# Optimization experiments

Hardware: AMD Instinct MI355X
Metric: run time of the kernel (lower is better)

## Reference

```python
import jax, jax.numpy as jnp
import numpy as np

M_CHANNELS = 256
N_KNOTS = 64
EPS = 1e-6


def setup_inputs() -> dict:
    key = jax.random.key(0)
    k_u, k_c = jax.random.split(key)
    u = jax.random.uniform(k_u, (4096, 64, M_CHANNELS), dtype=jnp.float32)
    # knots: per-channel sorted ascending, init linspace(0,1) as in the module
    knots = jnp.tile(jnp.linspace(0.0, 1.0, N_KNOTS, dtype=jnp.float32)[None, :],
                     (M_CHANNELS, 1))
    # coefs init to zeros in the module; use randn for a non-degenerate test
    coefs = jax.random.normal(k_c, (M_CHANNELS, N_KNOTS), dtype=jnp.float32)
    return {"u": u, "knots": knots, "coefs": coefs}


def reference(u, knots, coefs):
    """Piecewise-linear spline eval, vectorized over channels and points.
    u: [..., M], knots/coefs: [M, K] (knots sorted ascending per channel).
    """
    m, K = knots.shape
    orig_shape = u.shape
    flat = u.reshape(-1, m).T  # [M, N]
    # torch.bucketize(right=False) == searchsorted side='left'
    idx = jax.vmap(lambda k, x: jnp.searchsorted(k, x, side='left'))(knots, flat)
    idx0 = jnp.clip(idx - 1, 0, K - 2)  # [M, N]
    idx1 = idx0 + 1
    k0 = jnp.take_along_axis(knots, idx0, axis=1)
    k1 = jnp.take_along_axis(knots, idx1, axis=1)
    c0 = jnp.take_along_axis(coefs, idx0, axis=1)
    c1 = jnp.take_along_axis(coefs, idx1, axis=1)
    t = (flat - k0) / (k1 - k0 + EPS)
    out = c0 + t * (c1 - c0)  # [M, N]
    return out.T.reshape(orig_shape)
```

## Files before the change

### kernel.cpp

```cpp
#include <hip/hip_runtime.h>


#define EPS 1e-6f
#define NCH_GROUP 32
#define STRIDE 65
#define NGROUPS 8
#define BLOCKS_PER_GROUP 256
#define ROWS_PER_TILE 32

typedef float f32x4 __attribute__((ext_vector_type(4)));

__global__ __launch_bounds__(256, 8) void bspline_kernel(
    const float* __restrict__ u, const float* __restrict__ knots,
    const float* __restrict__ coefs, float* __restrict__ out, int n_rows)
{
    __shared__ float sK[NCH_GROUP * STRIDE];
    __shared__ float sC[NCH_GROUP * STRIDE];

    const int t = threadIdx.x;
    const int g = blockIdx.x & (NGROUPS - 1);
    const int b = blockIdx.x >> 3;

    const float* gk = knots + (size_t)g * NCH_GROUP * 64;
    const float* gc = coefs + (size_t)g * NCH_GROUP * 64;
    for (int i = t; i < NCH_GROUP * 64; i += 256) {
        int c = i >> 6;
        int k = i & 63;
        sK[c * STRIDE + k] = gk[i];
        sC[c * STRIDE + k] = gc[i];
    }
    __syncthreads();

    const int col4 = t & 7;
    const int rsub = t >> 3;
    const int lc = col4 * 4;

    float kmin[4], scale[4];
#pragma unroll
    for (int cc = 0; cc < 4; ++cc) {
        float klo = sK[(lc + cc) * STRIDE + 0];
        float khi = sK[(lc + cc) * STRIDE + 63];
        kmin[cc] = klo;
        scale[cc] = 63.0f * __builtin_amdgcn_rcpf(khi - klo);
    }

    const f32x4* u4 = (const f32x4*)u;
    f32x4* o4 = (f32x4*)out;
    const int colbase = g * 8 + col4;
    const int ntiles = n_rows / ROWS_PER_TILE;

    int rt = b;
    if (rt >= ntiles) return;
    size_t idx = (size_t)(rt * ROWS_PER_TILE + rsub) * 64 + colbase;
    f32x4 x4 = __builtin_nontemporal_load(&u4[idx]);

    for (;;) {
        const int rtn = rt + BLOCKS_PER_GROUP;
        const bool more = rtn < ntiles;
        size_t idxn = idx;
        f32x4 xn = x4;
        if (more) {
            idxn = (size_t)(rtn * ROWS_PER_TILE + rsub) * 64 + colbase;
            xn = __builtin_nontemporal_load(&u4[idxn]);
        }

        f32x4 r;
#pragma unroll
        for (int cc = 0; cc < 4; ++cc) {
            float x = x4[cc];
            const float* kp = &sK[(lc + cc) * STRIDE];
            const float* cp = &sC[(lc + cc) * STRIDE];

            float xs = (x - kmin[cc]) * scale[cc];
            int j = (int)xs;
            j = max(0, min(62, j));
            float k0 = kp[j];
            float k1 = kp[j + 1];
            while (j > 0 && k0 >= x) { --j; k1 = k0; k0 = kp[j]; }
            while (j < 62 && k1 < x) { ++j; k0 = k1; k1 = kp[j + 1]; }

            float tt = (x - k0) * __builtin_amdgcn_rcpf(k1 - k0 + EPS);
            float c0 = cp[j];
            float c1 = cp[j + 1];
            r[cc] = fmaf(tt, c1 - c0, c0);
        }
        __builtin_nontemporal_store(r, &o4[idx]);

        if (!more) break;
        rt = rtn; idx = idxn; x4 = xn;
    }
}

extern "C" void kernel_launch(void* const* d_in, const int* in_sizes, int n_in,
                              void* d_out, int out_size, void* d_ws, size_t ws_size,
                              hipStream_t stream) {
    const float* u     = (const float*)d_in[0];
    const float* knots = (const float*)d_in[1];
    const float* coefs = (const float*)d_in[2];
    float* out = (float*)d_out;

    int n_rows = in_sizes[0] / 256;

    dim3 grid(NGROUPS * BLOCKS_PER_GROUP);
    dim3 block(256);
    bspline_kernel<<<grid, block, 0, stream>>>(u, knots, coefs, out, n_rows);
}
```

Baseline: 443.1 us.

## Pack knot/coef segment pairs into float4 LDS and simplify row loop

Shared memory now holds one float4 per segment (k0, k1, c0, c1), so each lookup needs a single 128-bit LDS read instead of four scalar reads. The change also halves the blocks per channel group, drops the occupancy hint in the launch bounds, removes the manual software prefetch of the next tile, and replaces nontemporal loads and stores with ordinary ones. LDS use rises from about 16KB to 32KB per block, which can lower occupancy. The float4 reads with a 64-entry row stride may also cause bank conflicts, and the loop loses its explicit overlap of the next load with the current computation.

After: 450.2 us. Within noise of the previous version (+1.6%).

```diff
diff --git a/kernel.cpp b/kernel.cpp
--- a/kernel.cpp
+++ b/kernel.cpp
@@ -3,19 +3,17 @@
 
 #define EPS 1e-6f
 #define NCH_GROUP 32
-#define STRIDE 65
 #define NGROUPS 8
-#define BLOCKS_PER_GROUP 256
+#define BLOCKS_PER_GROUP 128
 #define ROWS_PER_TILE 32
 
 typedef float f32x4 __attribute__((ext_vector_type(4)));
 
-__global__ __launch_bounds__(256, 8) void bspline_kernel(
+__global__ __launch_bounds__(256) void bspline_kernel(
     const float* __restrict__ u, const float* __restrict__ knots,
     const float* __restrict__ coefs, float* __restrict__ out, int n_rows)
 {
-    __shared__ float sK[NCH_GROUP * STRIDE];
-    __shared__ float sC[NCH_GROUP * STRIDE];
+    __shared__ f32x4 sP[NCH_GROUP * 64];
 
     const int t = threadIdx.x;
     const int g = blockIdx.x & (NGROUPS - 1);
@@ -23,11 +21,15 @@
 
     const float* gk = knots + (size_t)g * NCH_GROUP * 64;
     const float* gc = coefs + (size_t)g * NCH_GROUP * 64;
-    for (int i = t; i < NCH_GROUP * 64; i += 256) {
-        int c = i >> 6;
-        int k = i & 63;
-        sK[c * STRIDE + k] = gk[i];
-        sC[c * STRIDE + k] = gc[i];
+    for (int i = t; i < NCH_GROUP * 63; i += 256) {
+        int c = i / 63;
+        int j = i - c * 63;
+        f32x4 p;
+        p.x = gk[c * 64 + j];
+        p.y = gk[c * 64 + j + 1];
+        p.z = gc[c * 64 + j];
+        p.w = gc[c * 64 + j + 1];
+        sP[(c << 6) + j] = p;
     }
     __syncthreads();
 
@@ -38,8 +40,8 @@
     float kmin[4], scale[4];
 #pragma unroll
     for (int cc = 0; cc < 4; ++cc) {
-        float klo = sK[(lc + cc) * STRIDE + 0];
-        float khi = sK[(lc + cc) * STRIDE + 63];
+        float klo = sP[(lc + cc) << 6].x;
+        float khi = sP[((lc + cc) << 6) + 62].y;
         kmin[cc] = klo;
         scale[cc] = 63.0f * __builtin_amdgcn_rcpf(khi - klo);
     }
@@ -49,45 +51,27 @@
     const int colbase = g * 8 + col4;
     const int ntiles = n_rows / ROWS_PER_TILE;
 
-    int rt = b;
-    if (rt >= ntiles) return;
-    size_t idx = (size_t)(rt * ROWS_PER_TILE + rsub) * 64 + colbase;
-    f32x4 x4 = __builtin_nontemporal_load(&u4[idx]);
-
-    for (;;) {
-        const int rtn = rt + BLOCKS_PER_GROUP;
-        const bool more = rtn < ntiles;
-        size_t idxn = idx;
-        f32x4 xn = x4;
-        if (more) {
-            idxn = (size_t)(rtn * ROWS_PER_TILE + rsub) * 64 + colbase;
-            xn = __builtin_nontemporal_load(&u4[idxn]);
-        }
-
+    for (int rt = b; rt < ntiles; rt += BLOCKS_PER_GROUP) {
+        int row = rt * ROWS_PER_TILE + rsub;
+        size_t idx = (size_t)row * 64 + colbase;
+        f32x4 x4 = u4[idx];
         f32x4 r;
 #pragma unroll
         for (int cc = 0; cc < 4; ++cc) {
             float x = x4[cc];
-            const float* kp = &sK[(lc + cc) * STRIDE];
-            const float* cp = &sC[(lc + cc) * STRIDE];
+            const f32x4* pc = &sP[(lc + cc) << 6];
 
             float xs = (x - kmin[cc]) * scale[cc];
             int j = (int)xs;
             j = max(0, min(62, j));
-            float k0 = kp[j];
-            float k1 = kp[j + 1];
-            while (j > 0 && k0 >= x) { --j; k1 = k0; k0 = kp[j]; }
-            while (j < 62 && k1 < x) { ++j; k0 = k1; k1 = kp[j + 1]; }
+            f32x4 p = pc[j];
+            while (j > 0 && p.x >= x) { --j; p = pc[j]; }
+            while (j < 62 && p.y < x) { ++j; p = pc[j]; }
 
-            float tt = (x - k0) * __builtin_amdgcn_rcpf(k1 - k0 + EPS);
-            float c0 = cp[j];
-            float c1 = cp[j + 1];
-            r[cc] = fmaf(tt, c1 - c0, c0);
+            float tt = (x - p.x) * __builtin_amdgcn_rcpf(p.y - p.x + EPS);
+            r[cc] = fmaf(tt, p.w - p.z, p.z);
         }
-        __builtin_nontemporal_store(r, &o4[idx]);
-
-        if (!more) break;
-        rt = rtn; idx = idxn; x4 = xn;
+        o4[idx] = r;
     }
 }
 
```
